# Kernel tuning notes

Measured on AMD Instinct MI355X. Metric: run time of the kernel, lower is better.

The kernel has to match this reference:

```python
import jax, jax.numpy as jnp
import numpy as np

B, T, C = 4, 2048, 1024
H = 16
HD = C // H  # 64


def setup_inputs() -> dict:
    key = jax.random.key(0)
    k1, k2, k3 = jax.random.split(key, 3)
    x = jax.random.normal(k1, (B, T, C), dtype=jnp.float32)
    W_qkv = jax.random.normal(k2, (3 * C, C), dtype=jnp.float32) * (C ** -0.5)
    W_proj = jax.random.normal(k3, (C, C), dtype=jnp.float32) * (C ** -0.5)
    b_proj = jnp.zeros((C,), dtype=jnp.float32)
    return {"x": x, "W_qkv": W_qkv, "W_proj": W_proj, "b_proj": b_proj}


def reference(x, W_qkv, W_proj, b_proj):
    # qkv = x @ W_qkv.T : [B,T,3C]
    qkv = jnp.einsum('btc,oc->bto', x, W_qkv)
    # Faithful to torch: view(B,T,H,3*HD) then chunk last dim -> per-head q/k/v
    qkv = qkv.reshape(B, T, H, 3 * HD)
    q, k, v = jnp.split(qkv, 3, axis=-1)      # each [B,T,H,HD]
    q = q.transpose(0, 2, 1, 3)               # [B,H,T,HD]
    k = k.transpose(0, 2, 1, 3)
    v = v.transpose(0, 2, 1, 3)
    scale = HD ** -0.5
    att = jnp.einsum('bhqd,bhkd->bhqk', q, k) * scale  # [B,H,T,T]
    causal = jnp.tril(jnp.ones((T, T), dtype=bool))
    att = jnp.where(causal, att, -jnp.inf)
    att = jax.nn.softmax(att, axis=-1)
    out = jnp.einsum('bhqk,bhkd->bhqd', att, v)        # [B,H,T,HD]
    out = out.transpose(0, 2, 1, 3).reshape(B, T, C)
    out = jnp.einsum('btc,oc->bto', out, W_proj) + b_proj
    return out
```

## Files before the change

### kernel.cpp

```cpp
#include <hip/hip_runtime.h>
#include <stdint.h>

#define B_ 4
#define T_ 2048
#define C_ 1024
#define H_ 16
#define HD_ 64

typedef __attribute__((ext_vector_type(8))) short short8;
typedef __attribute__((ext_vector_type(4))) float f32x4;

typedef uint32_t __attribute__((address_space(3))) lds_u32;
typedef const uint32_t __attribute__((address_space(1))) glb_u32;

__device__ inline void async16(const void* g, void* l) {
    __builtin_amdgcn_global_load_lds((glb_u32*)g, (lds_u32*)l, 16, 0, 0);
}

__device__ inline short f2bf(float f) {
    union { float f; uint32_t u; } x; x.f = f;
    uint32_t r = (x.u + 0x7fffu + ((x.u >> 16) & 1u)) >> 16;
    return (short)r;
}
__device__ inline float bf2f(short b) {
    union { uint32_t u; float f; } x; x.u = ((uint32_t)(uint16_t)b) << 16;
    return x.f;
}
__device__ inline uint32_t cvt_pk_bf16(float lo, float hi) {
    uint32_t r;
    asm("v_cvt_pk_bf16_f32 %0, %1, %2" : "=v"(r) : "v"(lo), "v"(hi));
    return r;
}

#define FENCE asm volatile("" ::: "memory")
#define BAR   do { FENCE; __builtin_amdgcn_s_barrier(); FENCE; } while (0)
#define VMC4  asm volatile("s_waitcnt vmcnt(4)" ::: "memory")

__global__ void convert_all(const void* __restrict__ x,  const void* __restrict__ wq,
                            const void* __restrict__ wp, const void* __restrict__ bias,
                            short* __restrict__ xd, short* __restrict__ wqd,
                            short* __restrict__ wpd, short* __restrict__ biasd,
                            int* __restrict__ flag_out)
{
    __shared__ int cnt;
    if (threadIdx.x == 0) cnt = 0;
    __syncthreads();
    int sane = 0;
    const uint32_t* xu = (const uint32_t*)x;
    for (int i = threadIdx.x; i < 1024; i += 256) {
        float v = bf2f((short)(xu[i] & 0xFFFFu));
        float a = fabsf(v);
        if (a > 1e-5f && a < 1e5f) sane++;
    }
    atomicAdd(&cnt, sane);
    __syncthreads();
    const int isf32 = (cnt < 512) ? 1 : 0;

    const int blk = blockIdx.x;
    const void* src; short* dst; int base, n;
    if (blk < 4096)      { src = x;    dst = xd;    base = blk;        n = B_*T_*C_; }
    else if (blk < 5632) { src = wq;   dst = wqd;   base = blk - 4096; n = 3*C_*C_; }
    else if (blk < 6144) { src = wp;   dst = wpd;   base = blk - 5632; n = C_*C_; }
    else                 { src = bias; dst = biasd; base = 0;          n = C_;
                           if (threadIdx.x == 0) *flag_out = isf32; }
    const int i = (base * 256 + threadIdx.x) * 8;
    if (i >= n) return;
    if (isf32) {
        const float* s = (const float*)src;
        short8 o;
#pragma unroll
        for (int j = 0; j < 8; j++) o[j] = f2bf(s[i + j]);
        *(short8*)&dst[i] = o;
    } else {
        *(short8*)&dst[i] = *(const short8*)((const short*)src + i);
    }
}

template <bool DUAL>
__global__ __launch_bounds__(512, 2) void gemm8(
    const short* __restrict__ A, const short* __restrict__ Bm,
    const short* __restrict__ bias_bf, void* __restrict__ Cout,
    int M, int N, int K, const int* __restrict__ flag)
{
    __shared__ short lds[65536];
    const int tid  = threadIdx.x;
    const int lane = tid & 63;
    const int wid  = tid >> 6;
    const int quad = lane >> 4;
    const int lcol = lane & 15;
    const int wm   = wid >> 2;
    const int wn   = wid & 3;
    const int nbx  = N >> 8;

    const int nwg = gridDim.x;
    const int qq = nwg >> 3, rr = nwg & 7;
    const int xcd = blockIdx.x & 7, lid = blockIdx.x >> 3;
    const int wg = (xcd < rr ? xcd * (qq + 1) : rr * (qq + 1) + (xcd - rr) * qq) + lid;
    const int m0 = (wg / nbx) << 8;
    const int n0 = (wg % nbx) << 8;
    const int isf32 = DUAL ? *flag : 0;

    const int srow = tid >> 3;
    const int sch  = ((tid & 7) ^ (srow & 7)) << 3;

    auto stageA = [&](int buf, int h, int kt) {
        const short* g = &A[(size_t)(m0 + srow + h * 64) * K + kt * 64 + sch];
        short* l = &lds[buf * 16384 + h * 8192 + tid * 8];
        async16(g, l);
        async16(g + (size_t)128 * K, l + 4096);
    };
    auto stageB = [&](int buf, int h, int kt) {
        const int br = (srow & 31) + ((srow >> 5) << 6) + h * 32;
        const short* g = &Bm[(size_t)(n0 + br) * K + kt * 64 + sch];
        short* l = &lds[32768 + buf * 16384 + h * 8192 + tid * 8];
        async16(g, l);
        async16(g + (size_t)128 * K, l + 4096);
    };

    f32x4 acc[8][4];
#pragma unroll
    for (int i = 0; i < 8; i++)
#pragma unroll
        for (int j = 0; j < 4; j++) acc[i][j] = f32x4{0.f, 0.f, 0.f, 0.f};

    short8 a0[8], a1[8], b0[4], b1[4];

    auto rdA = [&](short8* d, int buf, int qm) {
#pragma unroll
        for (int m2 = 0; m2 < 4; m2++)
#pragma unroll
            for (int ks = 0; ks < 2; ks++)
                d[m2 * 2 + ks] = *(const short8*)&lds[buf * 16384 + qm * 8192
                    + (wm * 64 + m2 * 16 + lcol) * 64
                    + ((((ks << 2) | quad) ^ (lcol & 7)) << 3)];
    };
    auto rdB = [&](short8* d, int buf, int qn) {
#pragma unroll
        for (int n2 = 0; n2 < 2; n2++)
#pragma unroll
            for (int ks = 0; ks < 2; ks++)
                d[n2 * 2 + ks] = *(const short8*)&lds[32768 + buf * 16384 + qn * 8192
                    + (wn * 32 + n2 * 16 + lcol) * 64
                    + ((((ks << 2) | quad) ^ (lcol & 7)) << 3)];
    };
    auto mm = [&](short8* a, short8* b, int qm, int qn) {
        __builtin_amdgcn_s_setprio(1);
#pragma unroll
        for (int m2 = 0; m2 < 4; m2++)
#pragma unroll
            for (int n2 = 0; n2 < 2; n2++)
#pragma unroll
                for (int ks = 0; ks < 2; ks++)
                    acc[qm * 4 + m2][qn * 2 + n2] = __builtin_amdgcn_mfma_f32_16x16x32_bf16(
                        a[m2 * 2 + ks], b[n2 * 2 + ks], acc[qm * 4 + m2][qn * 2 + n2], 0, 0, 0);
        __builtin_amdgcn_s_setprio(0);
    };

    const int NT = K >> 6;
    stageB(0, 0, 0); stageA(0, 0, 0); stageB(0, 1, 0); stageA(0, 1, 0);
    stageB(1, 0, 1); stageA(1, 0, 1);
    VMC4;
    BAR;

    for (int i = 0; i < NT / 2; i++) {
        const int to = 2 * i + 1;
        const int t2 = (2 * i + 2 < NT) ? 2 * i + 2 : NT - 1;
        const int t3 = (2 * i + 3 < NT) ? 2 * i + 3 : NT - 1;
        rdA(a0, 0, 0); rdB(b0, 0, 0);
        stageB(1, 1, to);
        BAR; mm(a0, b0, 0, 0); BAR;
        rdA(a1, 0, 1);
        stageA(1, 1, to);
        BAR; mm(a1, b0, 1, 0); BAR;
        rdB(b1, 0, 1);
        stageB(0, 0, t2);
        BAR; mm(a0, b1, 0, 1); BAR;
        stageA(0, 0, t2);
        BAR; mm(a1, b1, 1, 1); VMC4; BAR;
        rdA(a0, 1, 0); rdB(b0, 1, 0);
        stageB(0, 1, t2);
        BAR; mm(a0, b0, 0, 0); BAR;
        rdA(a1, 1, 1);
        stageA(0, 1, t2);
        BAR; mm(a1, b0, 1, 0); BAR;
        rdB(b1, 1, 1);
        stageB(1, 0, t3);
        BAR; mm(a0, b1, 0, 1); BAR;
        stageA(1, 0, t3);
        BAR; mm(a1, b1, 1, 1); VMC4; BAR;
    }

#pragma unroll
    for (int ni = 0; ni < 4; ni++) {
        const int col = n0 + wn * 64 + ni * 16 + lcol;
        const float bv = bias_bf ? bf2f(bias_bf[col]) : 0.f;
#pragma unroll
        for (int mi = 0; mi < 8; mi++) {
            const int row = m0 + wm * 128 + mi * 16 + quad * 4;
#pragma unroll
            for (int r = 0; r < 4; r++) {
                const float val = acc[mi][ni][r] + bv;
                const size_t off = (size_t)(row + r) * N + col;
                if (DUAL && isf32) ((float*)Cout)[off] = val;
                else               ((short*)Cout)[off] = f2bf(val);
            }
        }
    }
}

__global__ __launch_bounds__(256) void attn(const short* __restrict__ qkv,
                                            short* __restrict__ att)
{
    __shared__ short lds_k[64][72];
    __shared__ short lds_vt[64][68];

    const int tid  = threadIdx.x;
    const int lane = tid & 63;
    const int wave = tid >> 6;
    const int quad = lane >> 4;
    const int lcol = lane & 15;

    const int bh   = blockIdx.x & 63;
    const int j    = blockIdx.x >> 6;
    const int b    = bh >> 4;
    const int h    = bh & 15;

    const size_t rowstride = 3 * C_;
    const size_t bhbase = (size_t)b * T_ * rowstride + (size_t)h * (3 * HD_);

    const int kkey = tid >> 2;
    const int kdp  = (tid & 3) * 16;
    const int vkey = tid & 63;
    const int vkp  = (vkey & 0x23) | ((vkey & 0x0C) << 1) | ((vkey & 0x10) >> 2);
    const int vd0  = (tid >> 6) * 16;

    short8 vones;
#pragma unroll
    for (int i = 0; i < 8; i++) vones[i] = (short)0x3F80;

    const short* kp; const short* vp;
    short8 kA, kB, vA, vB;
    const size_t TILE_STEP = (size_t)64 * rowstride;
    auto load_init = [&]() {
        kp = &qkv[bhbase + (size_t)kkey * rowstride + HD_ + kdp];
        vp = &qkv[bhbase + (size_t)vkey * rowstride + 2 * HD_ + vd0];
    };
    auto load_tile = [&]() {
        kA = *(const short8*)kp;
        kB = *(const short8*)(kp + 8);
        vA = *(const short8*)vp;
        vB = *(const short8*)(vp + 8);
        kp += TILE_STEP; vp += TILE_STEP;
    };

    const float SC = 0.1803368801f;
    auto scale_frag = [&](short8 q) {
        short8 r;
#pragma unroll
        for (int i = 0; i < 8; i++) r[i] = f2bf(bf2f(q[i]) * SC);
        return r;
    };

    auto process_chunk = [&](int qblk, bool sync_first) {
        const int q0 = qblk * 128;
        const int qA = q0 + wave * 16;
        const int qB = q0 + 64 + wave * 16;

        short8 qfA0, qfA1, qfB0, qfB1;
        {
            const size_t ba = bhbase + (size_t)(qA + lcol) * rowstride + quad * 8;
            qfA0 = scale_frag(*(const short8*)&qkv[ba]);
            qfA1 = scale_frag(*(const short8*)&qkv[ba + 32]);
            const size_t bb = bhbase + (size_t)(qB + lcol) * rowstride + quad * 8;
            qfB0 = scale_frag(*(const short8*)&qkv[bb]);
            qfB1 = scale_frag(*(const short8*)&qkv[bb + 32]);
        }

        f32x4 oA[4], oB[4], oLA, oLB;
#pragma unroll
        for (int i = 0; i < 4; i++) { oA[i] = f32x4{0.f,0.f,0.f,0.f}; oB[i] = f32x4{0.f,0.f,0.f,0.f}; }
        oLA = f32x4{0.f,0.f,0.f,0.f}; oLB = f32x4{0.f,0.f,0.f,0.f};

        load_init();
        load_tile();

        const int LT = 2 * qblk + 1;
        for (int kt = 0; kt <= LT; ++kt) {
            if (kt || sync_first) __syncthreads();
            *(short8*)&lds_k[kkey][kdp]     = kA;
            *(short8*)&lds_k[kkey][kdp + 8] = kB;
#pragma unroll
            for (int jj = 0; jj < 8; jj++) {
                lds_vt[vd0 + jj][vkp]     = vA[jj];
                lds_vt[vd0 + 8 + jj][vkp] = vB[jj];
            }
            __syncthreads();
            if (kt < LT) load_tile();

            const int k0 = kt * 64;
            const bool doA = (kt < LT);

            f32x4 SA[4], SB[4];
#pragma unroll
            for (int t = 0; t < 4; t++) {
                const short8 kf0 = *(const short8*)&lds_k[t * 16 + lcol][quad * 8];
                const short8 kf1 = *(const short8*)&lds_k[t * 16 + lcol][32 + quad * 8];
                SB[t] = f32x4{0.f, 0.f, 0.f, 0.f};
                SB[t] = __builtin_amdgcn_mfma_f32_16x16x32_bf16(kf0, qfB0, SB[t], 0, 0, 0);
                SB[t] = __builtin_amdgcn_mfma_f32_16x16x32_bf16(kf1, qfB1, SB[t], 0, 0, 0);
                if (doA) {
                    SA[t] = f32x4{0.f, 0.f, 0.f, 0.f};
                    SA[t] = __builtin_amdgcn_mfma_f32_16x16x32_bf16(kf0, qfA0, SA[t], 0, 0, 0);
                    SA[t] = __builtin_amdgcn_mfma_f32_16x16x32_bf16(kf1, qfA1, SA[t], 0, 0, 0);
                }
            }

            short8 vf[4][2];
#pragma unroll
            for (int dt = 0; dt < 4; dt++) {
                vf[dt][0] = *(const short8*)&lds_vt[dt * 16 + lcol][quad * 8];
                vf[dt][1] = *(const short8*)&lds_vt[dt * 16 + lcol][32 + quad * 8];
            }

            auto do_mtile = [&](f32x4 (&S)[4], f32x4 (&o)[4], f32x4& oL,
                                int qX, bool maskT) {
                if (maskT) {
                    const int qthr = qX + lcol - k0 - quad * 4;
#pragma unroll
                    for (int t = 0; t < 4; t++)
#pragma unroll
                        for (int r = 0; r < 4; r++) {
                            float e = __builtin_amdgcn_exp2f(S[t][r]);
                            if (t * 16 + r > qthr) e = 0.f;
                            S[t][r] = e;
                        }
                } else {
#pragma unroll
                    for (int t = 0; t < 4; t++)
#pragma unroll
                        for (int r = 0; r < 4; r++)
                            S[t][r] = __builtin_amdgcn_exp2f(S[t][r]);
                }
                union { uint32_t u[4]; short8 s; } p0, p1;
#pragma unroll
                for (int w = 0; w < 4; w++) {
                    const int t0 = w >> 1, r0 = (w & 1) * 2;
                    p0.u[w] = cvt_pk_bf16(S[t0][r0],     S[t0][r0 + 1]);
                    p1.u[w] = cvt_pk_bf16(S[2 + t0][r0], S[2 + t0][r0 + 1]);
                }
                oL = __builtin_amdgcn_mfma_f32_16x16x32_bf16(p0.s, vones, oL, 0, 0, 0);
                oL = __builtin_amdgcn_mfma_f32_16x16x32_bf16(p1.s, vones, oL, 0, 0, 0);
#pragma unroll
                for (int dt = 0; dt < 4; dt++) {
                    o[dt] = __builtin_amdgcn_mfma_f32_16x16x32_bf16(p0.s, vf[dt][0], o[dt], 0, 0, 0);
                    o[dt] = __builtin_amdgcn_mfma_f32_16x16x32_bf16(p1.s, vf[dt][1], o[dt], 0, 0, 0);
                }
            };

            if (doA) do_mtile(SA, oA, oLA, qA, kt == LT - 1);
            do_mtile(SB, oB, oLB, qB, kt == LT);
        }

#pragma unroll
        for (int r = 0; r < 4; r++) {
            const float la = oLA[r], lb = oLB[r];
            const float iar = (la > 0.f) ? 1.f / la : 0.f;
            const float ibr = (lb > 0.f) ? 1.f / lb : 0.f;
            const int qi  = quad * 4 + r;
            const int qrA = qA + qi;
            const int qrB = qB + qi;
#pragma unroll
            for (int dt = 0; dt < 4; dt++) {
                const int col = h * HD_ + dt * 16 + lcol;
                att[(size_t)(b * T_ + qrA) * C_ + col] = f2bf(oA[dt][r] * iar);
                att[(size_t)(b * T_ + qrB) * C_ + col] = f2bf(oB[dt][r] * ibr);
            }
        }
    };

    process_chunk(15 - j, false);
    process_chunk(j, true);
}

extern "C" void kernel_launch(void* const* d_in, const int* in_sizes, int n_in,
                              void* d_out, int out_size, void* d_ws, size_t ws_size,
                              hipStream_t stream) {
    char* ws = (char*)d_ws;
    short* qkv     = (short*)(ws);
    short* x_or_at = (short*)(ws + 50331648);
    short* wq_bf   = (short*)(ws + 50331648 + 16777216);
    short* wp_bf   = (short*)(ws + 50331648 + 16777216 + 6291456);
    short* bias_bf = (short*)(ws + 50331648 + 16777216 + 6291456 + 2097152);
    int*   flag    = (int*)  (ws + 50331648 + 16777216 + 6291456 + 2097152 + 2048);

    dim3 blk(256);

    convert_all<<<dim3(6145), blk, 0, stream>>>(
        d_in[0], d_in[1], d_in[2], d_in[3],
        x_or_at, wq_bf, wp_bf, bias_bf, flag);

    gemm8<false><<<dim3(384), dim3(512), 0, stream>>>(
        x_or_at, wq_bf, nullptr, qkv, B_ * T_, 3 * C_, C_, flag);

    attn<<<dim3(B_ * H_ * (T_ / 256)), blk, 0, stream>>>(qkv, x_or_at);

    gemm8<true><<<dim3(128), dim3(512), 0, stream>>>(
        x_or_at, wp_bf, bias_bf, d_out, B_ * T_, C_, C_, flag);
}
```

Before: 253.7 us.

## Shrink GEMM block tile to 128x256 to double workgroup count

The GEMM tile is halved in M (256x256 to 128x256), so LDS use drops to 96KB and the per-wave accumulator to 4x4 fragments. The staging and MFMA schedule is rewritten to match, and the grid doubles (768 and 256 workgroups), giving better CU coverage on the 256-CU part, especially for the projection GEMM, which had only 128 blocks. The XCD remap is simplified to assume the grid divides evenly by 8. The cost is less data reuse per tile, so more global and L2 traffic per FLOP.

```diff
diff --git a/kernel.cpp b/kernel.cpp
--- a/kernel.cpp
+++ b/kernel.cpp
@@ -34,7 +34,7 @@
 
 #define FENCE asm volatile("" ::: "memory")
 #define BAR   do { FENCE; __builtin_amdgcn_s_barrier(); FENCE; } while (0)
-#define VMC4  asm volatile("s_waitcnt vmcnt(4)" ::: "memory")
+#define VMC3  asm volatile("s_waitcnt vmcnt(3)" ::: "memory")
 
 __global__ void convert_all(const void* __restrict__ x,  const void* __restrict__ wq,
                             const void* __restrict__ wp, const void* __restrict__ bias,
@@ -82,7 +82,7 @@
     const short* __restrict__ bias_bf, void* __restrict__ Cout,
     int M, int N, int K, const int* __restrict__ flag)
 {
-    __shared__ short lds[65536];
+    __shared__ short lds[49152];
     const int tid  = threadIdx.x;
     const int lane = tid & 63;
     const int wid  = tid >> 6;
@@ -92,120 +92,108 @@
     const int wn   = wid & 3;
     const int nbx  = N >> 8;
 
-    const int nwg = gridDim.x;
-    const int qq = nwg >> 3, rr = nwg & 7;
-    const int xcd = blockIdx.x & 7, lid = blockIdx.x >> 3;
-    const int wg = (xcd < rr ? xcd * (qq + 1) : rr * (qq + 1) + (xcd - rr) * qq) + lid;
-    const int m0 = (wg / nbx) << 8;
+    const int cpx = gridDim.x >> 3;
+    const int wg  = (blockIdx.x & 7) * cpx + (blockIdx.x >> 3);
+    const int m0 = (wg / nbx) << 7;
     const int n0 = (wg % nbx) << 8;
     const int isf32 = DUAL ? *flag : 0;
 
     const int srow = tid >> 3;
     const int sch  = ((tid & 7) ^ (srow & 7)) << 3;
-
-    auto stageA = [&](int buf, int h, int kt) {
-        const short* g = &A[(size_t)(m0 + srow + h * 64) * K + kt * 64 + sch];
-        short* l = &lds[buf * 16384 + h * 8192 + tid * 8];
-        async16(g, l);
-        async16(g + (size_t)128 * K, l + 4096);
-    };
-    auto stageB = [&](int buf, int h, int kt) {
-        const int br = (srow & 31) + ((srow >> 5) << 6) + h * 32;
-        const short* g = &Bm[(size_t)(n0 + br) * K + kt * 64 + sch];
-        short* l = &lds[32768 + buf * 16384 + h * 8192 + tid * 8];
-        async16(g, l);
-        async16(g + (size_t)128 * K, l + 4096);
-    };
-
-    f32x4 acc[8][4];
-#pragma unroll
-    for (int i = 0; i < 8; i++)
+    auto stA = [&](int buf, int i, int kt) {
+        async16(&A[(size_t)(m0 + i * 64 + srow) * K + kt * 64 + sch],
+                &lds[buf * 8192 + i * 4096 + tid * 8]);
+    };
+    auto stB = [&](int buf, int i, int kt) {
+        async16(&Bm[(size_t)(n0 + i * 64 + srow) * K + kt * 64 + sch],
+                &lds[16384 + buf * 16384 + i * 4096 + tid * 8]);
+    };
+
+    f32x4 acc[4][4];
+#pragma unroll
+    for (int i = 0; i < 4; i++)
 #pragma unroll
         for (int j = 0; j < 4; j++) acc[i][j] = f32x4{0.f, 0.f, 0.f, 0.f};
 
-    short8 a0[8], a1[8], b0[4], b1[4];
-
-    auto rdA = [&](short8* d, int buf, int qm) {
-#pragma unroll
-        for (int m2 = 0; m2 < 4; m2++)
+    short8 a[4][2], b[4][2];
+    auto rdA2 = [&](int mb, int buf) {
+#pragma unroll
+        for (int m2 = 0; m2 < 2; m2++)
 #pragma unroll
             for (int ks = 0; ks < 2; ks++)
-                d[m2 * 2 + ks] = *(const short8*)&lds[buf * 16384 + qm * 8192
-                    + (wm * 64 + m2 * 16 + lcol) * 64
+                a[mb + m2][ks] = *(const short8*)&lds[buf * 8192
+                    + (wm * 64 + (mb + m2) * 16 + lcol) * 64
                     + ((((ks << 2) | quad) ^ (lcol & 7)) << 3)];
     };
-    auto rdB = [&](short8* d, int buf, int qn) {
+    auto rdB2 = [&](int nb, int buf) {
 #pragma unroll
         for (int n2 = 0; n2 < 2; n2++)
 #pragma unroll
             for (int ks = 0; ks < 2; ks++)
-                d[n2 * 2 + ks] = *(const short8*)&lds[32768 + buf * 16384 + qn * 8192
-                    + (wn * 32 + n2 * 16 + lcol) * 64
+                b[nb + n2][ks] = *(const short8*)&lds[16384 + buf * 16384
+                    + (wn * 64 + (nb + n2) * 16 + lcol) * 64
                     + ((((ks << 2) | quad) ^ (lcol & 7)) << 3)];
     };
-    auto mm = [&](short8* a, short8* b, int qm, int qn) {
+    auto mmq = [&](int mb, int nb) {
         __builtin_amdgcn_s_setprio(1);
 #pragma unroll
-        for (int m2 = 0; m2 < 4; m2++)
+        for (int m2 = 0; m2 < 2; m2++)
 #pragma unroll
             for (int n2 = 0; n2 < 2; n2++)
 #pragma unroll
                 for (int ks = 0; ks < 2; ks++)
-                    acc[qm * 4 + m2][qn * 2 + n2] = __builtin_amdgcn_mfma_f32_16x16x32_bf16(
-                        a[m2 * 2 + ks], b[n2 * 2 + ks], acc[qm * 4 + m2][qn * 2 + n2], 0, 0, 0);
+                    acc[mb + m2][nb + n2] = __builtin_amdgcn_mfma_f32_16x16x32_bf16(
+                        a[mb + m2][ks], b[nb + n2][ks], acc[mb + m2][nb + n2], 0, 0, 0);
         __builtin_amdgcn_s_setprio(0);
     };
 
     const int NT = K >> 6;
-    stageB(0, 0, 0); stageA(0, 0, 0); stageB(0, 1, 0); stageA(0, 1, 0);
-    stageB(1, 0, 1); stageA(1, 0, 1);
-    VMC4;
+    stB(0, 0, 0); stB(0, 1, 0); stB(0, 2, 0); stB(0, 3, 0);
+    stA(0, 0, 0); stA(0, 1, 0);
+    stB(1, 0, 1); stB(1, 1, 1); stA(1, 0, 1);
+    VMC3;
     BAR;
 
     for (int i = 0; i < NT / 2; i++) {
         const int to = 2 * i + 1;
         const int t2 = (2 * i + 2 < NT) ? 2 * i + 2 : NT - 1;
         const int t3 = (2 * i + 3 < NT) ? 2 * i + 3 : NT - 1;
-        rdA(a0, 0, 0); rdB(b0, 0, 0);
-        stageB(1, 1, to);
-        BAR; mm(a0, b0, 0, 0); BAR;
-        rdA(a1, 0, 1);
-        stageA(1, 1, to);
-        BAR; mm(a1, b0, 1, 0); BAR;
-        rdB(b1, 0, 1);
-        stageB(0, 0, t2);
-        BAR; mm(a0, b1, 0, 1); BAR;
-        stageA(0, 0, t2);
-        BAR; mm(a1, b1, 1, 1); VMC4; BAR;
-        rdA(a0, 1, 0); rdB(b0, 1, 0);
-        stageB(0, 1, t2);
-        BAR; mm(a0, b0, 0, 0); BAR;
-        rdA(a1, 1, 1);
-        stageA(0, 1, t2);
-        BAR; mm(a1, b0, 1, 0); BAR;
-        rdB(b1, 1, 1);
-        stageB(1, 0, t3);
-        BAR; mm(a0, b1, 0, 1); BAR;
-        stageA(1, 0, t3);
-        BAR; mm(a1, b1, 1, 1); VMC4; BAR;
+        rdA2(0, 0); rdB2(0, 0); stB(1, 2, to); stB(1, 3, to);
+        BAR; mmq(0, 0); BAR;
+        rdA2(2, 0);             stA(1, 1, to);
+        BAR; mmq(2, 0); BAR;
+        rdB2(2, 0);
+        BAR; mmq(0, 2); BAR;
+        stB(0, 0, t2); stB(0, 1, t2); stA(0, 0, t2);
+        BAR; mmq(2, 2); VMC3; BAR;
+        rdA2(0, 1); rdB2(0, 1); stB(0, 2, t2); stB(0, 3, t2);
+        BAR; mmq(0, 0); BAR;
+        rdA2(2, 1);             stA(0, 1, t2);
+        BAR; mmq(2, 0); BAR;
+        rdB2(2, 1);
+        BAR; mmq(0, 2); BAR;
+        stB(1, 0, t3); stB(1, 1, t3); stA(1, 0, t3);
+        BAR; mmq(2, 2); VMC3; BAR;
     }
 
-#pragma unroll
-    for (int ni = 0; ni < 4; ni++) {
-        const int col = n0 + wn * 64 + ni * 16 + lcol;
-        const float bv = bias_bf ? bf2f(bias_bf[col]) : 0.f;
-#pragma unroll
-        for (int mi = 0; mi < 8; mi++) {
-            const int row = m0 + wm * 128 + mi * 16 + quad * 4;
-#pragma unroll
-            for (int r = 0; r < 4; r++) {
-                const float val = acc[mi][ni][r] + bv;
-                const size_t off = (size_t)(row + r) * N + col;
+    float bv[4];
+#pragma unroll
+    for (int nf = 0; nf < 4; nf++)
+        bv[nf] = bias_bf ? bf2f(bias_bf[n0 + wn * 64 + nf * 16 + lcol]) : 0.f;
+#pragma unroll
+    for (int mf = 0; mf < 4; mf++)
+#pragma unroll
+        for (int r = 0; r < 4; r++) {
+            const int row = m0 + wm * 64 + mf * 16 + quad * 4 + r;
+#pragma unroll
+            for (int nf = 0; nf < 4; nf++) {
+                const int col = n0 + wn * 64 + nf * 16 + lcol;
+                const float val = acc[mf][nf][r] + bv[nf];
+                const size_t off = (size_t)row * N + col;
                 if (DUAL && isf32) ((float*)Cout)[off] = val;
                 else               ((short*)Cout)[off] = f2bf(val);
             }
         }
-    }
 }
 
 __global__ __launch_bounds__(256) void attn(const short* __restrict__ qkv,
@@ -399,11 +387,11 @@
         d_in[0], d_in[1], d_in[2], d_in[3],
         x_or_at, wq_bf, wp_bf, bias_bf, flag);
 
-    gemm8<false><<<dim3(384), dim3(512), 0, stream>>>(
+    gemm8<false><<<dim3(768), dim3(512), 0, stream>>>(
         x_or_at, wq_bf, nullptr, qkv, B_ * T_, 3 * C_, C_, flag);
 
     attn<<<dim3(B_ * H_ * (T_ / 256)), blk, 0, stream>>>(qkv, x_or_at);
 
-    gemm8<true><<<dim3(128), dim3(512), 0, stream>>>(
+    gemm8<true><<<dim3(256), dim3(512), 0, stream>>>(
         x_or_at, wp_bf, bias_bf, d_out, B_ * T_, C_, C_, flag);
 }
```

Measured after the change: 252.0 us. About the same (-0.7%).
